# Performance work log

Measured on AMD Instinct MI355X. Metric: run time of the kernel, lower is better.

## Reference

```python
import jax, jax.numpy as jnp
import numpy as np

N = 400000
INC = 32
OUTC = 32
K = 27  # 3x3x3 kernel offsets
BN_EPS = 1e-5


def setup_inputs() -> dict:
    key = jax.random.key(0)
    ks = jax.random.split(key, 6)
    feats = jax.random.normal(ks[0], (N, INC), dtype=jnp.float32)
    kernel = jax.random.normal(ks[1], (K, INC, OUTC), dtype=jnp.float32) * 0.05
    bn_gamma = jnp.ones((OUTC,), dtype=jnp.float32)
    bn_beta = jnp.zeros((OUTC,), dtype=jnp.float32)
    bn_mean = jax.random.normal(ks[2], (OUTC,), dtype=jnp.float32) * 0.1
    bn_var = jax.random.uniform(ks[3], (OUTC,), dtype=jnp.float32) + 0.5
    in_idx = jax.random.randint(ks[4], (K, N), 0, N, dtype=jnp.int32)
    out_idx = jax.random.randint(ks[5], (K, N), 0, N, dtype=jnp.int32)
    return {"feats": feats, "kernel": kernel, "bn_gamma": bn_gamma,
            "bn_beta": bn_beta, "bn_mean": bn_mean, "bn_var": bn_var,
            "in_idx": in_idx, "out_idx": out_idx}


def _sparse_conv(feats, kernel, in_idx, out_idx):
    # gather -> per-offset matmul -> scatter-add, looped over the 27 offsets
    # via lax.scan to avoid materializing a [K, N, C] intermediate.
    out0 = jnp.zeros((feats.shape[0], kernel.shape[-1]), dtype=feats.dtype)

    def step(out, xs):
        w_k, iin, iout = xs  # [inc,outc], [M], [M]
        gathered = feats[iin]              # [M, inc]  irregular gather
        contrib = gathered @ w_k           # [M, outc] per-offset GEMM
        return out.at[iout].add(contrib), None  # scatter-accumulate

    out, _ = jax.lax.scan(step, out0, (kernel, in_idx, out_idx))
    return out


def reference(feats, kernel, bn_gamma, bn_beta, bn_mean, bn_var, in_idx, out_idx):
    out = _sparse_conv(feats, kernel, in_idx, out_idx)
    # BatchNorm (eval mode, running stats) over the feature dim
    inv_std = jax.lax.rsqrt(bn_var + BN_EPS)
    out = (out - bn_mean) * (bn_gamma * inv_std) + bn_beta
    # ReLU
    return jnp.maximum(out, 0.0)
```

## Files before the change

kernel.cpp:

```cpp
#include <hip/hip_runtime.h>
#include <hip/hip_bf16.h>
#include <hip/hip_fp16.h>

constexpr int INC  = 32;
constexpr int OUTC = 32;
constexpr int CHROWS  = 256;
constexpr int NSLICE  = 8;
constexpr int CAPB    = 384;
constexpr int CPS_MAX = 208;
constexpr int ACCW    = 17;

typedef __bf16 bf16x8 __attribute__((ext_vector_type(8)));
typedef float  f32x4  __attribute__((ext_vector_type(4)));
typedef __attribute__((address_space(3))) unsigned long long lds_u64;
typedef __attribute__((address_space(3))) unsigned           lds_u32;


__device__ __forceinline__ void lds_add_u64(unsigned long long* p,
                                            unsigned long long v) {
    __hip_atomic_fetch_add((lds_u64*)p, v,
                           __ATOMIC_RELAXED, __HIP_MEMORY_SCOPE_WORKGROUP);
}
__device__ __forceinline__ unsigned lds_add_u32(unsigned* p, unsigned v) {
    return __hip_atomic_fetch_add((lds_u32*)p, v,
                                  __ATOMIC_RELAXED, __HIP_MEMORY_SCOPE_WORKGROUP);
}

__device__ __forceinline__ unsigned long long enc2(float a, float b) {
    const int q0 = __float2int_rn(a * 65536.0f);
    const int q1 = __float2int_rn(b * 65536.0f);
    return (unsigned long long)((long long)q0 + ((long long)q1 << 32));
}

template<bool DO_PREP>
__global__ __launch_bounds__(1024) void fill_fused(
    const float* __restrict__ feats,
    __bf16*      __restrict__ fbf,
    const int*   __restrict__ in_idx,
    const int*   __restrict__ out_idx,
    unsigned* __restrict__ recsB,
    unsigned* __restrict__ cntB,
    int N, int cps, int slice_rows, int total8)
{
    __shared__ unsigned cur[CPS_MAX];
    const int s = blockIdx.x, k = blockIdx.y;
    const int tid = threadIdx.x;
    for (int c = tid; c < cps; c += 1024) cur[c] = 0u;

    if constexpr (DO_PREP) {
        const int nb    = gridDim.x * gridDim.y;
        const int b     = k * gridDim.x + s;
        const int share = (total8 + nb - 1) / nb;
        const int beg   = b * share;
        const int end   = min(total8, beg + share);
        for (int i = beg + tid; i < end; i += 1024) {
            const float4* p = (const float4*)(feats + (size_t)i * 8);
            const float4 a = p[0], bb = p[1];
            bf16x8 v;
            v[0] = (__bf16)a.x;  v[1] = (__bf16)a.y;
            v[2] = (__bf16)a.z;  v[3] = (__bf16)a.w;
            v[4] = (__bf16)bb.x; v[5] = (__bf16)bb.y;
            v[6] = (__bf16)bb.z; v[7] = (__bf16)bb.w;
            *(bf16x8*)(fbf + (size_t)i * 8) = v;
        }
    }
    __syncthreads();

    const int* iin_p  = in_idx  + (size_t)k * N;
    const int* iout_p = out_idx + (size_t)k * N;
    const int nchunkpad = NSLICE * cps;
    const unsigned lo = (unsigned)(s * slice_rows);
    const unsigned hi = lo + (unsigned)slice_rows;
    const size_t segbase = ((size_t)k * nchunkpad + (size_t)s * cps) * CAPB;

    for (int i0 = tid * 4; i0 < N; i0 += 4096) {
        const int4 ov = *(const int4*)(iout_p + i0);
        const int4 iv = *(const int4*)(iin_p + i0);
        const unsigned o[4]  = {(unsigned)ov.x, (unsigned)ov.y,
                                (unsigned)ov.z, (unsigned)ov.w};
        const unsigned ii[4] = {(unsigned)iv.x, (unsigned)iv.y,
                                (unsigned)iv.z, (unsigned)iv.w};
#pragma unroll
        for (int j = 0; j < 4; ++j) {
            if (o[j] >= lo && o[j] < hi) {
                const unsigned olo  = o[j] - lo;
                const unsigned c    = olo >> 8;
                const unsigned lrow = olo & 255u;
                const unsigned pos  = lds_add_u32(&cur[c], 1u);
                if (pos < (unsigned)CAPB)
                    recsB[segbase + (size_t)c * CAPB + pos] = ii[j] | (lrow << 19);
            }
        }
    }
    __syncthreads();
    for (int c = tid; c < cps; c += 1024)
        cntB[(size_t)k * nchunkpad + (size_t)s * cps + c] =
            min(cur[c], (unsigned)CAPB);
}

template<bool BF16F>
__global__ __launch_bounds__(576) void conv_chunk(
    const float*  __restrict__ feats,
    const __bf16* __restrict__ fbf,
    const float*  __restrict__ wkern,
    const unsigned* __restrict__ recsB,
    const unsigned* __restrict__ cntB,
    const float* __restrict__ gamma, const float* __restrict__ beta,
    const float* __restrict__ mean,  const float* __restrict__ var,
    float* __restrict__ out, int N, int nchunkpad)
{
    __shared__ unsigned long long accw[(CHROWS + 1) * ACCW];
    const int tid = threadIdx.x;
    for (int i = tid; i < (CHROWS + 1) * ACCW; i += 576) accw[i] = 0ull;
    __syncthreads();

    const int c    = blockIdx.x;
    const int wid  = tid >> 6;
    const int lane = tid & 63;
    const int col  = lane & 15;
    const int quad = lane >> 4;

#pragma unroll
    for (int kk = 0; kk < 3; ++kk) {
        const int k = wid + kk * 9;
        const int bidx = k * nchunkpad + c;
        const int cnt = (int)cntB[bidx];
        if (cnt == 0) continue;
        const unsigned* seg = recsB + (size_t)bidx * CAPB;

        const float* wk = wkern + (size_t)k * (INC * OUTC);
        bf16x8 b0, b1;
#pragma unroll
        for (int j = 0; j < 8; ++j) {
            const float2 w2 = *(const float2*)(wk + (quad * 8 + j) * OUTC + 2 * col);
            b0[j] = (__bf16)w2.x;
            b1[j] = (__bf16)w2.y;
        }

        const int ntile = (cnt + 15) >> 4;

        auto do_tile = [&](int t) {
            const int sbase = t << 4;
            const unsigned ra = seg[sbase + col];
            const unsigned iidx = (sbase + col < cnt) ? (ra & 0x7FFFFu) : 0u;
            bf16x8 a;
            if constexpr (BF16F) {
                a = *(const bf16x8*)(fbf + (size_t)iidx * INC + quad * 8);
            } else {
                const float4* ap = (const float4*)(feats + (size_t)iidx * INC + quad * 8);
                const float4 alo = ap[0], ahi = ap[1];
                a[0] = (__bf16)alo.x; a[1] = (__bf16)alo.y;
                a[2] = (__bf16)alo.z; a[3] = (__bf16)alo.w;
                a[4] = (__bf16)ahi.x; a[5] = (__bf16)ahi.y;
                a[6] = (__bf16)ahi.z; a[7] = (__bf16)ahi.w;
            }
            const uint4 rv = *(const uint4*)(seg + sbase + quad * 4);
            f32x4 acc0 = {0.f, 0.f, 0.f, 0.f};
            f32x4 acc1 = {0.f, 0.f, 0.f, 0.f};
            acc0 = __builtin_amdgcn_mfma_f32_16x16x32_bf16(a, b0, acc0, 0, 0, 0);
            acc1 = __builtin_amdgcn_mfma_f32_16x16x32_bf16(a, b1, acc1, 0, 0, 0);
            const unsigned rr[4] = { rv.x, rv.y, rv.z, rv.w };
#pragma unroll
            for (int r = 0; r < 4; ++r) {
                const int idx  = sbase + quad * 4 + r;
                const int lrow = (idx < cnt) ? (int)((rr[r] >> 19) & 255u) : CHROWS;
                lds_add_u64(&accw[lrow * ACCW + col], enc2(acc0[r], acc1[r]));
            }
        };

        int t = 0;
        for (; t + 2 <= ntile; t += 2) {
            const int s0 = t << 4, s1 = s0 + 16;
            const unsigned ra0 = seg[s0 + col];
            const unsigned ra1 = seg[s1 + col];
            const uint4 rv0 = *(const uint4*)(seg + s0 + quad * 4);
            const uint4 rv1 = *(const uint4*)(seg + s1 + quad * 4);
            const unsigned i0 = (s0 + col < cnt) ? (ra0 & 0x7FFFFu) : 0u;
            const unsigned i1 = (s1 + col < cnt) ? (ra1 & 0x7FFFFu) : 0u;

            bf16x8 a0, a1;
            if constexpr (BF16F) {
                a0 = *(const bf16x8*)(fbf + (size_t)i0 * INC + quad * 8);
                a1 = *(const bf16x8*)(fbf + (size_t)i1 * INC + quad * 8);
            } else {
                const float4* p0 = (const float4*)(feats + (size_t)i0 * INC + quad * 8);
                const float4* p1 = (const float4*)(feats + (size_t)i1 * INC + quad * 8);
                const float4 a0lo = p0[0], a0hi = p0[1];
                const float4 a1lo = p1[0], a1hi = p1[1];
                a0[0] = (__bf16)a0lo.x; a0[1] = (__bf16)a0lo.y;
                a0[2] = (__bf16)a0lo.z; a0[3] = (__bf16)a0lo.w;
                a0[4] = (__bf16)a0hi.x; a0[5] = (__bf16)a0hi.y;
                a0[6] = (__bf16)a0hi.z; a0[7] = (__bf16)a0hi.w;
                a1[0] = (__bf16)a1lo.x; a1[1] = (__bf16)a1lo.y;
                a1[2] = (__bf16)a1lo.z; a1[3] = (__bf16)a1lo.w;
                a1[4] = (__bf16)a1hi.x; a1[5] = (__bf16)a1hi.y;
                a1[6] = (__bf16)a1hi.z; a1[7] = (__bf16)a1hi.w;
            }

            f32x4 c00 = {0.f, 0.f, 0.f, 0.f};
            f32x4 c01 = {0.f, 0.f, 0.f, 0.f};
            f32x4 c10 = {0.f, 0.f, 0.f, 0.f};
            f32x4 c11 = {0.f, 0.f, 0.f, 0.f};
            c00 = __builtin_amdgcn_mfma_f32_16x16x32_bf16(a0, b0, c00, 0, 0, 0);
            c01 = __builtin_amdgcn_mfma_f32_16x16x32_bf16(a0, b1, c01, 0, 0, 0);
            c10 = __builtin_amdgcn_mfma_f32_16x16x32_bf16(a1, b0, c10, 0, 0, 0);
            c11 = __builtin_amdgcn_mfma_f32_16x16x32_bf16(a1, b1, c11, 0, 0, 0);

            const unsigned rr0[4] = { rv0.x, rv0.y, rv0.z, rv0.w };
            const unsigned rr1[4] = { rv1.x, rv1.y, rv1.z, rv1.w };
#pragma unroll
            for (int r = 0; r < 4; ++r) {
                const int idx0  = s0 + quad * 4 + r;
                const int lrow0 = (idx0 < cnt) ? (int)((rr0[r] >> 19) & 255u) : CHROWS;
                lds_add_u64(&accw[lrow0 * ACCW + col], enc2(c00[r], c01[r]));
            }
#pragma unroll
            for (int r = 0; r < 4; ++r) {
                const int idx1  = s1 + quad * 4 + r;
                const int lrow1 = (idx1 < cnt) ? (int)((rr1[r] >> 19) & 255u) : CHROWS;
                lds_add_u64(&accw[lrow1 * ACCW + col], enc2(c10[r], c11[r]));
            }
        }
        for (; t < ntile; ++t) do_tile(t);
    }
    __syncthreads();

    if (tid < 512) {
        const int p  = tid & 15;
        const int c0 = 2 * p;
        const int r0 = tid >> 4;
        const float s0 = gamma[c0]     * rsqrtf(var[c0]     + 1e-5f);
        const float s1 = gamma[c0 + 1] * rsqrtf(var[c0 + 1] + 1e-5f);
        const float q0 = beta[c0]     - mean[c0]     * s0;
        const float q1 = beta[c0 + 1] - mean[c0 + 1] * s1;
#pragma unroll
        for (int it = 0; it < CHROWS / 32; ++it) {
            const int row  = it * 32 + r0;
            const int grow = c * CHROWS + row;
            if (grow < N) {
                long long t = (long long)accw[row * ACCW + p];
                const int d0 = (int)(unsigned)(t & 0xFFFFFFFFll);
                const int d1 = (int)((t - (long long)d0) >> 32);
                float2 o;
                o.x = fmaxf(fmaf((float)d0 * (1.f / 65536.f), s0, q0), 0.f);
                o.y = fmaxf(fmaf((float)d1 * (1.f / 65536.f), s1, q1), 0.f);
                *(float2*)(out + (size_t)grow * OUTC + c0) = o;
            }
        }
    }
}

__global__ __launch_bounds__(256) void scatter_conv_mfma_pk(
    const float* __restrict__ feats,
    const float* __restrict__ wkern,
    const int*   __restrict__ in_idx,
    const int*   __restrict__ out_idx,
    __half2*     __restrict__ ws,
    int N)
{
    const int k    = blockIdx.y;
    const int lane = threadIdx.x & 63;
    const int col  = lane & 15;
    const int quad = lane >> 4;

    const int wave   = blockIdx.x * 4 + (threadIdx.x >> 6);
    const int nwaves = gridDim.x * 4;

    const float* wk = wkern + (size_t)k * (INC * OUTC);
    bf16x8 b0, b1;
#pragma unroll
    for (int j = 0; j < 8; ++j) {
        const int kk = quad * 8 + j;
        b0[j] = (__bf16)wk[kk * OUTC + 2 * col];
        b1[j] = (__bf16)wk[kk * OUTC + 2 * col + 1];
    }

    const int* iin_p  = in_idx  + (size_t)k * N;
    const int* iout_p = out_idx + (size_t)k * N;
    const int  ntiles = N >> 4;

    for (int t = wave; t < ntiles; t += nwaves) {
        const int base = t << 4;
        const int iin = iin_p[base + col];
        int orow[4];
#pragma unroll
        for (int r = 0; r < 4; ++r) orow[r] = iout_p[base + quad * 4 + r];

        const float4* ap = (const float4*)(feats + (size_t)iin * INC + quad * 8);
        const float4 a_lo = ap[0];
        const float4 a_hi = ap[1];
        bf16x8 a;
        a[0] = (__bf16)a_lo.x; a[1] = (__bf16)a_lo.y;
        a[2] = (__bf16)a_lo.z; a[3] = (__bf16)a_lo.w;
        a[4] = (__bf16)a_hi.x; a[5] = (__bf16)a_hi.y;
        a[6] = (__bf16)a_hi.z; a[7] = (__bf16)a_hi.w;

        f32x4 acc0 = {0.f, 0.f, 0.f, 0.f};
        f32x4 acc1 = {0.f, 0.f, 0.f, 0.f};
        acc0 = __builtin_amdgcn_mfma_f32_16x16x32_bf16(a, b0, acc0, 0, 0, 0);
        acc1 = __builtin_amdgcn_mfma_f32_16x16x32_bf16(a, b1, acc1, 0, 0, 0);

#pragma unroll
        for (int r = 0; r < 4; ++r) {
            __half2 v = __halves2half2(__float2half(acc0[r]), __float2half(acc1[r]));
            unsafeAtomicAdd(ws + (size_t)orow[r] * 16 + col, v);
        }
    }
}

__global__ __launch_bounds__(256) void bn_relu_f16(
    const __half2* __restrict__ ws,
    float* __restrict__ out,
    const float* __restrict__ gamma,
    const float* __restrict__ beta,
    const float* __restrict__ mean,
    const float* __restrict__ var,
    int total2)
{
    const int tid    = blockIdx.x * blockDim.x + threadIdx.x;
    const int stride = gridDim.x * blockDim.x;
    const int p      = tid & 15;
    const int c0     = 2 * p;

    float s0 = gamma[c0]     * rsqrtf(var[c0]     + 1e-5f);
    float s1 = gamma[c0 + 1] * rsqrtf(var[c0 + 1] + 1e-5f);
    float q0 = beta[c0]     - mean[c0]     * s0;
    float q1 = beta[c0 + 1] - mean[c0 + 1] * s1;

    float2* po = (float2*)out;
    for (int i = tid; i < total2; i += stride) {
        const __half2 h = ws[i];
        float2 v;
        v.x = fmaxf(fmaf(__low2float(h),  s0, q0), 0.0f);
        v.y = fmaxf(fmaf(__high2float(h), s1, q1), 0.0f);
        po[i] = v;
    }
}

__global__ __launch_bounds__(256) void scatter_conv_mfma_f32(
    const float* __restrict__ feats,
    const float* __restrict__ wkern,
    const int*   __restrict__ in_idx,
    const int*   __restrict__ out_idx,
    float*       __restrict__ out,
    int N)
{
    const int k    = blockIdx.y;
    const int lane = threadIdx.x & 63;
    const int col  = lane & 15;
    const int quad = lane >> 4;
    const int wave   = blockIdx.x * 4 + (threadIdx.x >> 6);
    const int nwaves = gridDim.x * 4;

    const float* wk = wkern + (size_t)k * (INC * OUTC);
    bf16x8 b0, b1;
#pragma unroll
    for (int j = 0; j < 8; ++j) {
        const int kk = quad * 8 + j;
        b0[j] = (__bf16)wk[kk * OUTC + col];
        b1[j] = (__bf16)wk[kk * OUTC + 16 + col];
    }

    const int* iin_p  = in_idx  + (size_t)k * N;
    const int* iout_p = out_idx + (size_t)k * N;
    const int  ntiles = N >> 4;

    for (int t = wave; t < ntiles; t += nwaves) {
        const int base = t << 4;
        const int iin = iin_p[base + col];
        int orow[4];
#pragma unroll
        for (int r = 0; r < 4; ++r) orow[r] = iout_p[base + quad * 4 + r];

        const float4* ap = (const float4*)(feats + (size_t)iin * INC + quad * 8);
        const float4 a_lo = ap[0];
        const float4 a_hi = ap[1];
        bf16x8 a;
        a[0] = (__bf16)a_lo.x; a[1] = (__bf16)a_lo.y;
        a[2] = (__bf16)a_lo.z; a[3] = (__bf16)a_lo.w;
        a[4] = (__bf16)a_hi.x; a[5] = (__bf16)a_hi.y;
        a[6] = (__bf16)a_hi.z; a[7] = (__bf16)a_hi.w;

        f32x4 acc0 = {0.f, 0.f, 0.f, 0.f};
        f32x4 acc1 = {0.f, 0.f, 0.f, 0.f};
        acc0 = __builtin_amdgcn_mfma_f32_16x16x32_bf16(a, b0, acc0, 0, 0, 0);
        acc1 = __builtin_amdgcn_mfma_f32_16x16x32_bf16(a, b1, acc1, 0, 0, 0);

#pragma unroll
        for (int r = 0; r < 4; ++r) {
            float* dst = out + (size_t)orow[r] * OUTC + col;
            unsafeAtomicAdd(dst,      acc0[r]);
            unsafeAtomicAdd(dst + 16, acc1[r]);
        }
    }
}

__global__ __launch_bounds__(256) void bn_relu_f32_inplace(
    float* __restrict__ out,
    const float* __restrict__ gamma,
    const float* __restrict__ beta,
    const float* __restrict__ mean,
    const float* __restrict__ var,
    int total4)
{
    const int tid    = blockIdx.x * blockDim.x + threadIdx.x;
    const int stride = gridDim.x * blockDim.x;
    const int c0     = (tid & 7) << 2;

    float s[4], b[4];
#pragma unroll
    for (int j = 0; j < 4; ++j) {
        const int c = c0 + j;
        s[j] = gamma[c] * rsqrtf(var[c] + 1e-5f);
        b[j] = beta[c] - mean[c] * s[j];
    }

    float4* p = (float4*)out;
    for (int i = tid; i < total4; i += stride) {
        float4 v = p[i];
        v.x = fmaxf(fmaf(v.x, s[0], b[0]), 0.0f);
        v.y = fmaxf(fmaf(v.y, s[1], b[1]), 0.0f);
        v.z = fmaxf(fmaf(v.z, s[2], b[2]), 0.0f);
        v.w = fmaxf(fmaf(v.w, s[3], b[3]), 0.0f);
        p[i] = v;
    }
}

extern "C" void kernel_launch(void* const* d_in, const int* in_sizes, int n_in,
                              void* d_out, int out_size, void* d_ws, size_t ws_size,
                              hipStream_t stream) {
    const float* feats   = (const float*)d_in[0];
    const float* wkern   = (const float*)d_in[1];
    const float* gamma   = (const float*)d_in[2];
    const float* beta    = (const float*)d_in[3];
    const float* mean    = (const float*)d_in[4];
    const float* var     = (const float*)d_in[5];
    const int*   in_idx  = (const int*)d_in[6];
    const int*   out_idx = (const int*)d_in[7];
    float*       out     = (float*)d_out;

    const int N = in_sizes[0] / INC;
    const int K = in_sizes[1] / (INC * OUTC);

    const int nchunk     = (N + CHROWS - 1) / CHROWS;
    const int cps        = (nchunk + NSLICE - 1) / NSLICE;
    const int nchunkpad  = NSLICE * cps;
    const int slice_rows = cps * CHROWS;

    auto al = [](size_t x) { return (x + 255) & ~(size_t)255; };
    size_t off = 0;
    const size_t cntB_off  = off; off = al(off + (size_t)K * nchunkpad * 4);
    const size_t recsB_off = off; off = al(off + (size_t)K * nchunkpad * CAPB * 4);
    const size_t need_core = off;
    const size_t fbf_off   = off;
    const size_t need_full = off + al((size_t)N * INC * 2);
    const size_t need_pk   = (size_t)N * OUTC * sizeof(__half);

    const bool chunk_ok = (N <= (1 << 19)) && (N % 4 == 0) &&
                          (cps <= CPS_MAX) && (K == 27);

    if (chunk_ok && ws_size >= need_core) {
        char* base = (char*)d_ws;
        unsigned* cntB  = (unsigned*)(base + cntB_off);
        unsigned* recsB = (unsigned*)(base + recsB_off);

        const bool use_bf16 = ws_size >= need_full;
        if (use_bf16) {
            __bf16* fbf = (__bf16*)(base + fbf_off);
            fill_fused<true><<<dim3(NSLICE, K), 1024, 0, stream>>>(
                feats, fbf, in_idx, out_idx, recsB, cntB,
                N, cps, slice_rows, N * 4);
            conv_chunk<true><<<nchunk, 576, 0, stream>>>(
                feats, fbf, wkern, recsB, cntB, gamma, beta, mean, var,
                out, N, nchunkpad);
        } else {
            fill_fused<false><<<dim3(NSLICE, K), 1024, 0, stream>>>(
                feats, nullptr, in_idx, out_idx, recsB, cntB,
                N, cps, slice_rows, N * 4);
            conv_chunk<false><<<nchunk, 576, 0, stream>>>(
                feats, nullptr, wkern, recsB, cntB, gamma, beta, mean, var,
                out, N, nchunkpad);
        }
    } else if (ws_size >= need_pk) {
        __half2* acc = (__half2*)d_ws;
        hipMemsetAsync(acc, 0, need_pk, stream);
        dim3 grid(80, K);
        scatter_conv_mfma_pk<<<grid, 256, 0, stream>>>(
            feats, wkern, in_idx, out_idx, acc, N);
        bn_relu_f16<<<1024, 256, 0, stream>>>(acc, out, gamma, beta, mean, var, N * 16);
    } else {
        hipMemsetAsync(out, 0, (size_t)out_size * sizeof(float), stream);
        dim3 grid(80, K);
        scatter_conv_mfma_f32<<<grid, 256, 0, stream>>>(
            feats, wkern, in_idx, out_idx, out, N);
        bn_relu_f32_inplace<<<1024, 256, 0, stream>>>(
            out, gamma, beta, mean, var, out_size / 4);
    }
}
```

Measured before the change: 551.8 us.

## Bucket records with global atomics over input partitions instead of slice-filtered scans

The fill stage previously had each of 8 slices per offset scan the full index arrays and keep only entries in its output range, counting with LDS atomics. Now each of 32 partitions per offset reads only its own share of the indices and bumps per-chunk counters in global memory with atomics, after a memset of the counters. This removes the eightfold redundant index reading, at the cost of contended global atomics and an extra memset launch. The conv kernel now clamps counts to capacity because the counters can exceed it.

```diff
diff --git a/kernel.cpp b/kernel.cpp
--- a/kernel.cpp
+++ b/kernel.cpp
@@ -5,15 +5,13 @@
 constexpr int INC  = 32;
 constexpr int OUTC = 32;
 constexpr int CHROWS  = 256;
-constexpr int NSLICE  = 8;
+constexpr int NPARTF  = 32;
 constexpr int CAPB    = 384;
-constexpr int CPS_MAX = 208;
 constexpr int ACCW    = 17;
 
 typedef __bf16 bf16x8 __attribute__((ext_vector_type(8)));
 typedef float  f32x4  __attribute__((ext_vector_type(4)));
 typedef __attribute__((address_space(3))) unsigned long long lds_u64;
-typedef __attribute__((address_space(3))) unsigned           lds_u32;
 
 
 __device__ __forceinline__ void lds_add_u64(unsigned long long* p,
@@ -21,10 +19,6 @@
     __hip_atomic_fetch_add((lds_u64*)p, v,
                            __ATOMIC_RELAXED, __HIP_MEMORY_SCOPE_WORKGROUP);
 }
-__device__ __forceinline__ unsigned lds_add_u32(unsigned* p, unsigned v) {
-    return __hip_atomic_fetch_add((lds_u32*)p, v,
-                                  __ATOMIC_RELAXED, __HIP_MEMORY_SCOPE_WORKGROUP);
-}
 
 __device__ __forceinline__ unsigned long long enc2(float a, float b) {
     const int q0 = __float2int_rn(a * 65536.0f);
@@ -33,29 +27,27 @@
 }
 
 template<bool DO_PREP>
-__global__ __launch_bounds__(1024) void fill_fused(
+__global__ __launch_bounds__(256) void fill_dense(
     const float* __restrict__ feats,
     __bf16*      __restrict__ fbf,
     const int*   __restrict__ in_idx,
     const int*   __restrict__ out_idx,
     unsigned* __restrict__ recsB,
     unsigned* __restrict__ cntB,
-    int N, int cps, int slice_rows, int total8)
-{
-    __shared__ unsigned cur[CPS_MAX];
-    const int s = blockIdx.x, k = blockIdx.y;
+    int N, int nchunkpad, int total8)
+{
+    const int p = blockIdx.x, k = blockIdx.y;
     const int tid = threadIdx.x;
-    for (int c = tid; c < cps; c += 1024) cur[c] = 0u;
 
     if constexpr (DO_PREP) {
         const int nb    = gridDim.x * gridDim.y;
-        const int b     = k * gridDim.x + s;
+        const int b     = k * gridDim.x + p;
         const int share = (total8 + nb - 1) / nb;
         const int beg   = b * share;
         const int end   = min(total8, beg + share);
-        for (int i = beg + tid; i < end; i += 1024) {
-            const float4* p = (const float4*)(feats + (size_t)i * 8);
-            const float4 a = p[0], bb = p[1];
+        for (int i = beg + tid; i < end; i += 256) {
+            const float4* fp = (const float4*)(feats + (size_t)i * 8);
+            const float4 a = fp[0], bb = fp[1];
             bf16x8 v;
             v[0] = (__bf16)a.x;  v[1] = (__bf16)a.y;
             v[2] = (__bf16)a.z;  v[3] = (__bf16)a.w;
@@ -64,38 +56,32 @@
             *(bf16x8*)(fbf + (size_t)i * 8) = v;
         }
     }
-    __syncthreads();
-
+
+    const int part_n = N / NPARTF;
+    const int ibeg   = p * part_n;
+    const int iend   = ibeg + part_n;
     const int* iin_p  = in_idx  + (size_t)k * N;
     const int* iout_p = out_idx + (size_t)k * N;
-    const int nchunkpad = NSLICE * cps;
-    const unsigned lo = (unsigned)(s * slice_rows);
-    const unsigned hi = lo + (unsigned)slice_rows;
-    const size_t segbase = ((size_t)k * nchunkpad + (size_t)s * cps) * CAPB;
-
-    for (int i0 = tid * 4; i0 < N; i0 += 4096) {
+    unsigned* ctr = cntB  + (size_t)k * nchunkpad;
+    unsigned* seg = recsB + (size_t)k * nchunkpad * CAPB;
+
+    for (int i0 = ibeg + tid * 4; i0 < iend; i0 += 1024) {
         const int4 ov = *(const int4*)(iout_p + i0);
         const int4 iv = *(const int4*)(iin_p + i0);
         const unsigned o[4]  = {(unsigned)ov.x, (unsigned)ov.y,
                                 (unsigned)ov.z, (unsigned)ov.w};
         const unsigned ii[4] = {(unsigned)iv.x, (unsigned)iv.y,
                                 (unsigned)iv.z, (unsigned)iv.w};
-#pragma unroll
-        for (int j = 0; j < 4; ++j) {
-            if (o[j] >= lo && o[j] < hi) {
-                const unsigned olo  = o[j] - lo;
-                const unsigned c    = olo >> 8;
-                const unsigned lrow = olo & 255u;
-                const unsigned pos  = lds_add_u32(&cur[c], 1u);
-                if (pos < (unsigned)CAPB)
-                    recsB[segbase + (size_t)c * CAPB + pos] = ii[j] | (lrow << 19);
-            }
-        }
-    }
-    __syncthreads();
-    for (int c = tid; c < cps; c += 1024)
-        cntB[(size_t)k * nchunkpad + (size_t)s * cps + c] =
-            min(cur[c], (unsigned)CAPB);
+        unsigned pos[4];
+#pragma unroll
+        for (int j = 0; j < 4; ++j)
+            pos[j] = atomicAdd(ctr + (o[j] >> 8), 1u);
+#pragma unroll
+        for (int j = 0; j < 4; ++j)
+            if (pos[j] < (unsigned)CAPB)
+                seg[(size_t)(o[j] >> 8) * CAPB + pos[j]]
+                    = ii[j] | ((o[j] & 255u) << 19);
+    }
 }
 
 template<bool BF16F>
@@ -124,7 +110,7 @@
     for (int kk = 0; kk < 3; ++kk) {
         const int k = wid + kk * 9;
         const int bidx = k * nchunkpad + c;
-        const int cnt = (int)cntB[bidx];
+        const int cnt = min((int)cntB[bidx], CAPB);
         if (cnt == 0) continue;
         const unsigned* seg = recsB + (size_t)bidx * CAPB;
 
@@ -442,10 +428,8 @@
     const int N = in_sizes[0] / INC;
     const int K = in_sizes[1] / (INC * OUTC);
 
-    const int nchunk     = (N + CHROWS - 1) / CHROWS;
-    const int cps        = (nchunk + NSLICE - 1) / NSLICE;
-    const int nchunkpad  = NSLICE * cps;
-    const int slice_rows = cps * CHROWS;
+    const int nchunk    = (N + CHROWS - 1) / CHROWS;
+    const int nchunkpad = (nchunk + 31) & ~31;
 
     auto al = [](size_t x) { return (x + 255) & ~(size_t)255; };
     size_t off = 0;
@@ -456,27 +440,27 @@
     const size_t need_full = off + al((size_t)N * INC * 2);
     const size_t need_pk   = (size_t)N * OUTC * sizeof(__half);
 
-    const bool chunk_ok = (N <= (1 << 19)) && (N % 4 == 0) &&
-                          (cps <= CPS_MAX) && (K == 27);
+    const bool chunk_ok = (N <= (1 << 19)) && (N % (NPARTF * 4) == 0) &&
+                          (nchunk <= 2048) && (K == 27);
 
     if (chunk_ok && ws_size >= need_core) {
         char* base = (char*)d_ws;
         unsigned* cntB  = (unsigned*)(base + cntB_off);
         unsigned* recsB = (unsigned*)(base + recsB_off);
 
+        hipMemsetAsync(cntB, 0, (size_t)K * nchunkpad * 4, stream);
+
         const bool use_bf16 = ws_size >= need_full;
         if (use_bf16) {
             __bf16* fbf = (__bf16*)(base + fbf_off);
-            fill_fused<true><<<dim3(NSLICE, K), 1024, 0, stream>>>(
-                feats, fbf, in_idx, out_idx, recsB, cntB,
-                N, cps, slice_rows, N * 4);
+            fill_dense<true><<<dim3(NPARTF, K), 256, 0, stream>>>(
+                feats, fbf, in_idx, out_idx, recsB, cntB, N, nchunkpad, N * 4);
             conv_chunk<true><<<nchunk, 576, 0, stream>>>(
                 feats, fbf, wkern, recsB, cntB, gamma, beta, mean, var,
                 out, N, nchunkpad);
         } else {
-            fill_fused<false><<<dim3(NSLICE, K), 1024, 0, stream>>>(
-                feats, nullptr, in_idx, out_idx, recsB, cntB,
-                N, cps, slice_rows, N * 4);
+            fill_dense<false><<<dim3(NPARTF, K), 256, 0, stream>>>(
+                feats, nullptr, in_idx, out_idx, recsB, cntB, N, nchunkpad, N * 4);
             conv_chunk<false><<<nchunk, 576, 0, stream>>>(
                 feats, nullptr, wkern, recsB, cntB, gamma, beta, mean, var,
                 out, N, nchunkpad);
```

New measurement: 917.6 us. +66.3%, slower.
